# Performance work log

Hardware: AMD Instinct MI355X
Metric: run time of the kernel (lower is better)

Reference implementation:

```python
import jax, jax.numpy as jnp
import numpy as np

N_RAYS = 4096
WORLD_LEN = 160
K0_DIM = 12
WIDTH = 128
VIEWPE = 4
BG_LEN = 0.2
XYZ_MIN = -1.0 - BG_LEN
XYZ_MAX = 1.0 + BG_LEN
ALPHA_INIT = 1e-4
ACT_SHIFT = float(np.log(1.0 / (1.0 - ALPHA_INIT) - 1.0))  # density bias shift
BG = 1.0  # background color (render_kwargs['bg'])
DIM0 = 3 + 3 * VIEWPE * 2 + K0_DIM  # 39


def grid_interp(grid, pts):
    """Trilinear interpolation (align_corners=True). grid: [C,R,R,R], pts: [M,3] world coords -> [M,C]."""
    R = grid.shape[1]
    g = (pts - XYZ_MIN) / (XYZ_MAX - XYZ_MIN) * (R - 1)
    g = jnp.clip(g, 0.0, R - 1)
    g0 = jnp.clip(jnp.floor(g).astype(jnp.int32), 0, R - 2)
    f = g - g0
    x0, y0, z0 = g0[:, 0], g0[:, 1], g0[:, 2]
    fx, fy, fz = f[:, 0], f[:, 1], f[:, 2]

    def gat(i, j, k):
        return grid[:, i, j, k]  # [C, M]

    c00 = gat(x0, y0, z0) * (1 - fz) + gat(x0, y0, z0 + 1) * fz
    c01 = gat(x0, y0 + 1, z0) * (1 - fz) + gat(x0, y0 + 1, z0 + 1) * fz
    c10 = gat(x0 + 1, y0, z0) * (1 - fz) + gat(x0 + 1, y0, z0 + 1) * fz
    c11 = gat(x0 + 1, y0 + 1, z0) * (1 - fz) + gat(x0 + 1, y0 + 1, z0 + 1) * fz
    c0 = c00 * (1 - fy) + c01 * fy
    c1 = c10 * (1 - fy) + c11 * fy
    return (c0 * (1 - fx) + c1 * fx).T  # [M, C]


def setup_inputs() -> dict:
    key = jax.random.key(0)
    ks = jax.random.split(key, 11)
    return {
        "rays_o": jax.random.normal(ks[0], (N_RAYS, 3), jnp.float32) * 0.3,
        "rays_d": jax.random.normal(ks[1], (N_RAYS, 3), jnp.float32),
        "viewdirs": jax.random.normal(ks[2], (N_RAYS, 3), jnp.float32),
        "density_grid": jax.random.normal(ks[3], (1, WORLD_LEN, WORLD_LEN, WORLD_LEN), jnp.float32),
        "k0_grid": jax.random.normal(ks[4], (K0_DIM, WORLD_LEN, WORLD_LEN, WORLD_LEN), jnp.float32),
        "w0": jax.random.normal(ks[5], (DIM0, WIDTH), jnp.float32) * 0.05,
        "b0": jnp.zeros((WIDTH,), jnp.float32),
        "w1": jax.random.normal(ks[6], (WIDTH, WIDTH), jnp.float32) * 0.05,
        "b1": jnp.zeros((WIDTH,), jnp.float32),
        "w2": jax.random.normal(ks[7], (WIDTH, 3), jnp.float32) * 0.05,
        "b2": jnp.zeros((3,), jnp.float32),
        "stepsize": 1,
    }


def reference(rays_o, rays_d, viewdirs, density_grid, k0_grid, w0, b0, w1, b1, w2, b2, stepsize):
    sqrt3 = float(np.sqrt(3.0))
    # --- sample_ray: sample points along rays in the contracted domain ---
    N_inner = int(2.0 / (2.0 + 2.0 * BG_LEN) * sqrt3 * WORLD_LEN / stepsize) + 1
    N_outer = int(N_inner * max(0.01, BG_LEN / 2.0))
    b_inner = jnp.linspace(0.0, 2.0 * sqrt3, N_inner + 1)
    b_outer = 2.0 * sqrt3 / jnp.linspace(1.0, 0.001, N_outer + 1)
    t = jnp.concatenate([(b_inner[1:] + b_inner[:-1]) * 0.5,
                         (b_outer[1:] + b_outer[:-1]) * 0.5])  # [P]
    # scene_center = 0, scene_radius = 1 for xyz_min=-1, xyz_max=1
    rd = rays_d / jnp.linalg.norm(rays_d, axis=-1, keepdims=True)
    pts = rays_o[:, None, :] + rd[:, None, :] * t[None, :, None]  # [N,P,3]
    norm = jnp.max(jnp.abs(pts), axis=-1, keepdims=True)
    safe = jnp.maximum(norm, 1e-9)
    pts = jnp.where(norm <= 1.0, pts, pts / safe * (1.0 + BG_LEN - BG_LEN / safe))
    N, P = pts.shape[0], pts.shape[1]
    flat = pts.reshape(-1, 3)  # [M,3]

    # --- density -> alpha (Raw2Alpha); mask_cache is all-True, fast_color_thres=0 ---
    interval = float(stepsize) * 1.0  # voxel_size_ratio == 1
    dens = grid_interp(density_grid, flat)[:, 0].reshape(N, P)
    alpha = 1.0 - jnp.power(1.0 + jnp.exp(dens + ACT_SHIFT), -interval)

    # --- Alphas2Weights: per-ray alpha compositing ---
    T = jnp.cumprod(1.0 - alpha, axis=1)
    T_excl = jnp.concatenate([jnp.ones((N, 1), T.dtype), T[:, :-1]], axis=1)
    weights = alpha * T_excl  # [N,P]
    alphainv_last = T[:, -1]  # [N]

    # --- k0 features + view-dependent MLP ---
    k0 = grid_interp(k0_grid, flat).reshape(N, P, K0_DIM)
    vf = (2.0 ** jnp.arange(VIEWPE)).astype(rays_o.dtype)
    ve = (viewdirs[..., None] * vf).reshape(N, -1)
    vemb = jnp.concatenate([viewdirs, jnp.sin(ve), jnp.cos(ve)], axis=-1)  # [N, 3+24]
    feat = jnp.concatenate(
        [k0, jnp.broadcast_to(vemb[:, None, :], (N, P, vemb.shape[-1]))], axis=-1)  # [N,P,39]
    h = jax.nn.relu(feat @ w0 + b0)
    h = jax.nn.relu(h @ w1 + b1)
    rgb = jax.nn.sigmoid(h @ w2 + b2)  # [N,P,3]

    # --- volume rendering ---
    rgb_marched = jnp.sum(weights[..., None] * rgb, axis=1) + alphainv_last[:, None] * BG
    return rgb_marched  # [N,3]
```

## Files before the change

### kernel.cpp

```cpp
#include <hip/hip_runtime.h>

#define NRAYS 4096
#define PSAMP 254
#define NIN   231
#define GR    160
#define GR2   25600
#define GR3   4096000
#define SROW  136

typedef __attribute__((ext_vector_type(8))) short bf16x8;
typedef __attribute__((ext_vector_type(4))) float f32x4;

__device__ __forceinline__ unsigned short f2bf(float x) {
    union { float f; unsigned u; } v; v.f = x;
    return (unsigned short)((v.u + 0x7fffu + ((v.u >> 16) & 1u)) >> 16);
}
__device__ __forceinline__ float sigmoidf_(float x) { return 1.0f / (1.0f + __expf(-x)); }

__global__ void prepack(const float* __restrict__ w, unsigned short* __restrict__ out,
                        int K, int N, int ldw, int NT, int KS) {
    const int idx = blockIdx.x * 256 + threadIdx.x;
    if (idx >= NT * KS * 64) return;
    const int l  = idx & 63, f = idx >> 6;
    const int ks = f % KS,  nt = f / KS;
    const int n  = nt * 16 + (l & 15);
    const int k0 = ks * 32 + (l >> 4) * 8;
    unsigned p[4];
    #pragma unroll
    for (int q = 0; q < 4; q++) {
        const int ka = k0 + 2 * q, kb = ka + 1;
        const float va = (ka < K && n < N) ? w[ka * ldw + n] : 0.0f;
        const float vb = (kb < K && n < N) ? w[kb * ldw + n] : 0.0f;
        p[q] = (unsigned)f2bf(va) | ((unsigned)f2bf(vb) << 16);
    }
    uint4 v; v.x = p[0]; v.y = p[1]; v.z = p[2]; v.w = p[3];
    ((uint4*)out)[idx] = v;
}

__global__ __launch_bounds__(256, 2) void voxgo_mfma(
    const float* __restrict__ rays_o, const float* __restrict__ rays_d,
    const float* __restrict__ viewdirs, const float* __restrict__ dg,
    const float* __restrict__ k0g,
    const float* __restrict__ b0, const float* __restrict__ b1,
    const float* __restrict__ b2,
    const unsigned short* __restrict__ pw0, const unsigned short* __restrict__ pw1,
    const unsigned short* __restrict__ pw2,
    float* __restrict__ out)
{
    const int r    = blockIdx.x;
    const int tid  = threadIdx.x;
    const int wv   = tid >> 6, lane = tid & 63, quad = lane >> 4, l16 = lane & 15;

    __shared__ unsigned short hbuf[4][64 * SROW];
    __shared__ float sc[256];
    __shared__ float wgt[256];
    __shared__ float redbuf[256];

    const float ox = rays_o[3*r+0], oy = rays_o[3*r+1], oz = rays_o[3*r+2];
    float dxv = rays_d[3*r+0], dyv = rays_d[3*r+1], dzv = rays_d[3*r+2];
    const float vdx = viewdirs[3*r+0], vdy = viewdirs[3*r+1], vdz = viewdirs[3*r+2];
    const float rinv = rsqrtf(dxv*dxv + dyv*dyv + dzv*dzv);
    dxv *= rinv; dyv *= rinv; dzv *= rinv;

    float t;
    if (tid < NIN) {
        t = ((float)tid + 0.5f) * (2.0f * 1.7320508075688772f / 231.0f);
    } else {
        const float lstep = 0.999f / 23.0f;
        const int j = tid - NIN;
        const float L0 = 1.0f - (float)j * lstep;
        const float L1 = 1.0f - (float)(j+1) * lstep;
        t = 1.7320508075688772f * (1.0f/L0 + 1.0f/L1);
    }

    float px = fmaf(dxv, t, ox), py = fmaf(dyv, t, oy), pz = fmaf(dzv, t, oz);
    const float nrm = fmaxf(fabsf(px), fmaxf(fabsf(py), fabsf(pz)));
    if (nrm > 1.0f) {
        const float s = (1.2f - 0.2f / nrm) / nrm;
        px *= s; py *= s; pz *= s;
    }

    const float gsc = 159.0f / 2.4f;
    const float gx = fminf(fmaxf((px + 1.2f) * gsc, 0.0f), 159.0f);
    const float gy = fminf(fmaxf((py + 1.2f) * gsc, 0.0f), 159.0f);
    const float gz = fminf(fmaxf((pz + 1.2f) * gsc, 0.0f), 159.0f);
    const int x0 = min((int)gx, GR-2), y0 = min((int)gy, GR-2), z0 = min((int)gz, GR-2);
    const float fx = gx - (float)x0, fy = gy - (float)y0, fz = gz - (float)z0;
    const int base = x0*GR2 + y0*GR + z0;

    const float d000 = dg[base],        d001 = dg[base+1];
    const float d010 = dg[base+GR],     d011 = dg[base+GR+1];
    const float d100 = dg[base+GR2],    d101 = dg[base+GR2+1];
    const float d110 = dg[base+GR2+GR], d111 = dg[base+GR2+GR+1];
    const float c00 = d000*(1.0f-fz) + d001*fz;
    const float c01 = d010*(1.0f-fz) + d011*fz;
    const float c10 = d100*(1.0f-fz) + d101*fz;
    const float c11 = d110*(1.0f-fz) + d111*fz;
    const float dens = (c00*(1.0f-fy) + c01*fy)*(1.0f-fx) + (c10*(1.0f-fy) + c11*fy)*fx;

    const float ACT_SHIFT = -9.21024036697535f;
    const float alpha = (tid < PSAMP) ? sigmoidf_(dens + ACT_SHIFT) : 0.0f;

    sc[tid] = 1.0f - alpha;
    __syncthreads();
    #pragma unroll
    for (int off = 1; off < 256; off <<= 1) {
        const float v = (tid >= off) ? sc[tid - off] : 1.0f;
        __syncthreads();
        sc[tid] *= v;
        __syncthreads();
    }
    const float T_excl = (tid == 0) ? 1.0f : sc[tid-1];
    wgt[tid] = alpha * T_excl;

    const float wx0 = 1.0f-fx, wy0 = 1.0f-fy, wz0 = 1.0f-fz;
    const float w000 = wx0*wy0*wz0, w001 = wx0*wy0*fz, w010 = wx0*fy*wz0, w011 = wx0*fy*fz;
    const float w100 = fx*wy0*wz0,  w101 = fx*wy0*fz,  w110 = fx*fy*wz0,  w111 = fx*fy*fz;

    float fv[40];
    #pragma unroll
    for (int c = 0; c < 12; c++) {
        const float* g = k0g + c*GR3 + base;
        fv[c] = w000*g[0]      + w001*g[1]
              + w010*g[GR]     + w011*g[GR+1]
              + w100*g[GR2]    + w101*g[GR2+1]
              + w110*g[GR2+GR] + w111*g[GR2+GR+1];
    }
    fv[12] = vdx; fv[13] = vdy; fv[14] = vdz;
    #pragma unroll
    for (int p = 0; p < 4; p++) {
        const float f = (float)(1 << p);
        fv[15+p] = __sinf(vdx*f);  fv[19+p] = __sinf(vdy*f);  fv[23+p] = __sinf(vdz*f);
        fv[27+p] = __cosf(vdx*f);  fv[31+p] = __cosf(vdy*f);  fv[35+p] = __cosf(vdz*f);
    }
    fv[39] = 0.0f;

    unsigned short* hb = &hbuf[wv][0];
    {
        const int row = tid & 63;
        uint4* dst = (uint4*)(hb + row * SROW);
        #pragma unroll
        for (int i = 0; i < 8; i++) {
            unsigned p[4];
            #pragma unroll
            for (int q = 0; q < 4; q++) {
                const int e0 = i*8 + 2*q, e1 = e0 + 1;
                const unsigned lo = (e0 < 39) ? f2bf(fv[e0]) : 0u;
                const unsigned hi = (e1 < 39) ? f2bf(fv[e1]) : 0u;
                p[q] = lo | (hi << 16);
            }
            uint4 v; v.x = p[0]; v.y = p[1]; v.z = p[2]; v.w = p[3];
            dst[i] = v;
        }
    }
    __syncthreads();


    f32x4 acc1[4][8];
    #pragma unroll
    for (int nt = 0; nt < 8; nt++) {
        const float bz = b0[nt*16 + l16];
        #pragma unroll
        for (int mt = 0; mt < 4; mt++) { f32x4 z = {bz,bz,bz,bz}; acc1[mt][nt] = z; }
    }
    #pragma unroll
    for (int ks = 0; ks < 2; ks++) {
        bf16x8 a[4];
        #pragma unroll
        for (int mt = 0; mt < 4; mt++)
            a[mt] = *(const bf16x8*)(hb + (mt*16 + l16)*SROW + ks*32 + quad*8);
        #pragma unroll
        for (int nt = 0; nt < 8; nt++) {
            const bf16x8 b = *(const bf16x8*)(pw0 + ((nt*2 + ks)*64 + lane)*8);
            #pragma unroll
            for (int mt = 0; mt < 4; mt++)
                acc1[mt][nt] = __builtin_amdgcn_mfma_f32_16x16x32_bf16(a[mt], b, acc1[mt][nt], 0,0,0);
        }
    }
    #pragma unroll
    for (int mt = 0; mt < 4; mt++)
        #pragma unroll
        for (int nt = 0; nt < 8; nt++)
            #pragma unroll
            for (int e = 0; e < 4; e++)
                hb[(mt*16 + quad*4 + e)*SROW + nt*16 + l16] = f2bf(fmaxf(acc1[mt][nt][e], 0.0f));
    __syncthreads();

    f32x4 acc2[4][8];
    #pragma unroll
    for (int nt = 0; nt < 8; nt++) {
        const float bz = b1[nt*16 + l16];
        #pragma unroll
        for (int mt = 0; mt < 4; mt++) { f32x4 z = {bz,bz,bz,bz}; acc2[mt][nt] = z; }
    }
    #pragma unroll
    for (int ks = 0; ks < 4; ks++) {
        bf16x8 a[4];
        #pragma unroll
        for (int mt = 0; mt < 4; mt++)
            a[mt] = *(const bf16x8*)(hb + (mt*16 + l16)*SROW + ks*32 + quad*8);
        #pragma unroll
        for (int nt = 0; nt < 8; nt++) {
            const bf16x8 b = *(const bf16x8*)(pw1 + ((nt*4 + ks)*64 + lane)*8);
            #pragma unroll
            for (int mt = 0; mt < 4; mt++)
                acc2[mt][nt] = __builtin_amdgcn_mfma_f32_16x16x32_bf16(a[mt], b, acc2[mt][nt], 0,0,0);
        }
    }
    #pragma unroll
    for (int mt = 0; mt < 4; mt++)
        #pragma unroll
        for (int nt = 0; nt < 8; nt++)
            #pragma unroll
            for (int e = 0; e < 4; e++)
                hb[(mt*16 + quad*4 + e)*SROW + nt*16 + l16] = f2bf(fmaxf(acc2[mt][nt][e], 0.0f));
    __syncthreads();

    f32x4 acc3[4];
    {
        const float bz = (l16 < 3) ? b2[l16] : 0.0f;
        #pragma unroll
        for (int mt = 0; mt < 4; mt++) { f32x4 z = {bz,bz,bz,bz}; acc3[mt] = z; }
    }
    #pragma unroll
    for (int ks = 0; ks < 4; ks++) {
        const bf16x8 b = *(const bf16x8*)(pw2 + (ks*64 + lane)*8);
        #pragma unroll
        for (int mt = 0; mt < 4; mt++) {
            const bf16x8 a = *(const bf16x8*)(hb + (mt*16 + l16)*SROW + ks*32 + quad*8);
            acc3[mt] = __builtin_amdgcn_mfma_f32_16x16x32_bf16(a, b, acc3[mt], 0,0,0);
        }
    }

    float contrib = 0.0f;
    #pragma unroll
    for (int mt = 0; mt < 4; mt++)
        #pragma unroll
        for (int e = 0; e < 4; e++) {
            const float s = sigmoidf_(acc3[mt][e]);
            contrib += wgt[wv*64 + mt*16 + quad*4 + e] * s;
        }
    redbuf[tid] = contrib;
    __syncthreads();
    if (tid < 3) {
        float acc_o = sc[PSAMP-1];
        #pragma unroll
        for (int w = 0; w < 4; w++)
            #pragma unroll
            for (int q = 0; q < 4; q++)
                acc_o += redbuf[w*64 + q*16 + tid];
        out[3*r + tid] = acc_o;
    }
}

extern "C" void kernel_launch(void* const* d_in, const int* in_sizes, int n_in,
                              void* d_out, int out_size, void* d_ws, size_t ws_size,
                              hipStream_t stream) {
    (void)in_sizes; (void)n_in; (void)out_size; (void)ws_size;
    unsigned short* pw0 = (unsigned short*)d_ws;
    unsigned short* pw1 = pw0 + 16*64*8;
    unsigned short* pw2 = pw1 + 32*64*8;

    prepack<<<4, 256, 0, stream>>>((const float*)d_in[5], pw0,  39, 128, 128, 8, 2);
    prepack<<<8, 256, 0, stream>>>((const float*)d_in[7], pw1, 128, 128, 128, 8, 4);
    prepack<<<1, 256, 0, stream>>>((const float*)d_in[9], pw2, 128,   3,   3, 1, 4);

    voxgo_mfma<<<NRAYS, 256, 0, stream>>>(
        (const float*)d_in[0],
        (const float*)d_in[1],
        (const float*)d_in[2],
        (const float*)d_in[3],
        (const float*)d_in[4],
        (const float*)d_in[6],
        (const float*)d_in[8],
        (const float*)d_in[10],
        pw0, pw1, pw2,
        (float*)d_out);
}
```

Baseline: 526.0 us.

## Split fused kernel into k0 repack, gather, and MLP kernels via workspace

```diff
diff --git a/kernel.cpp b/kernel.cpp
--- a/kernel.cpp
+++ b/kernel.cpp
@@ -7,6 +7,7 @@
 #define GR2   25600
 #define GR3   4096000
 #define SROW  136
+#define FROW  48
 
 typedef __attribute__((ext_vector_type(8))) short bf16x8;
 typedef __attribute__((ext_vector_type(4))) float f32x4;
@@ -14,6 +15,11 @@
 __device__ __forceinline__ unsigned short f2bf(float x) {
     union { float f; unsigned u; } v; v.f = x;
     return (unsigned short)((v.u + 0x7fffu + ((v.u >> 16) & 1u)) >> 16);
+}
+__device__ __forceinline__ float bfhalf(unsigned w, int hi) {
+    union { unsigned u; float f; } v;
+    v.u = hi ? (w & 0xffff0000u) : (w << 16);
+    return v.f;
 }
 __device__ __forceinline__ float sigmoidf_(float x) { return 1.0f / (1.0f + __expf(-x)); }
 
@@ -35,6 +41,238 @@
     }
     uint4 v; v.x = p[0]; v.y = p[1]; v.z = p[2]; v.w = p[3];
     ((uint4*)out)[idx] = v;
+}
+
+__global__ __launch_bounds__(256) void pack_k0(const float* __restrict__ k0g,
+                                               unsigned short* __restrict__ pk) {
+    const int v = blockIdx.x * 256 + threadIdx.x;
+    if (v >= GR3) return;
+    unsigned d[8];
+    #pragma unroll
+    for (int c = 0; c < 6; c++) {
+        const float a = k0g[(size_t)(2*c  ) * GR3 + v];
+        const float b = k0g[(size_t)(2*c+1) * GR3 + v];
+        d[c] = (unsigned)f2bf(a) | ((unsigned)f2bf(b) << 16);
+    }
+    d[6] = 0u; d[7] = 0u;
+    uint4* o = (uint4*)(pk + (size_t)v * 16);
+    uint4 v0; v0.x = d[0]; v0.y = d[1]; v0.z = d[2]; v0.w = d[3];
+    uint4 v1; v1.x = d[4]; v1.y = d[5]; v1.z = d[6]; v1.w = d[7];
+    o[0] = v0; o[1] = v1;
+}
+
+__global__ __launch_bounds__(256) void voxgo_gather(
+    const float* __restrict__ rays_o, const float* __restrict__ rays_d,
+    const float* __restrict__ viewdirs, const float* __restrict__ dg,
+    const unsigned short* __restrict__ pk0,
+    unsigned short* __restrict__ feat, float* __restrict__ wgt,
+    float* __restrict__ out)
+{
+    const int r = blockIdx.x, tid = threadIdx.x;
+    __shared__ float sc[256];
+
+    const float ox = rays_o[3*r+0], oy = rays_o[3*r+1], oz = rays_o[3*r+2];
+    float dxv = rays_d[3*r+0], dyv = rays_d[3*r+1], dzv = rays_d[3*r+2];
+    const float vdx = viewdirs[3*r+0], vdy = viewdirs[3*r+1], vdz = viewdirs[3*r+2];
+    const float rinv = rsqrtf(dxv*dxv + dyv*dyv + dzv*dzv);
+    dxv *= rinv; dyv *= rinv; dzv *= rinv;
+
+    float t;
+    if (tid < NIN) {
+        t = ((float)tid + 0.5f) * (2.0f * 1.7320508075688772f / 231.0f);
+    } else {
+        const float lstep = 0.999f / 23.0f;
+        const int j = tid - NIN;
+        const float L0 = 1.0f - (float)j * lstep;
+        const float L1 = 1.0f - (float)(j+1) * lstep;
+        t = 1.7320508075688772f * (1.0f/L0 + 1.0f/L1);
+    }
+
+    float px = fmaf(dxv, t, ox), py = fmaf(dyv, t, oy), pz = fmaf(dzv, t, oz);
+    const float nrm = fmaxf(fabsf(px), fmaxf(fabsf(py), fabsf(pz)));
+    if (nrm > 1.0f) {
+        const float s = (1.2f - 0.2f / nrm) / nrm;
+        px *= s; py *= s; pz *= s;
+    }
+    const float gsc = 159.0f / 2.4f;
+    const float gx = fminf(fmaxf((px + 1.2f) * gsc, 0.0f), 159.0f);
+    const float gy = fminf(fmaxf((py + 1.2f) * gsc, 0.0f), 159.0f);
+    const float gz = fminf(fmaxf((pz + 1.2f) * gsc, 0.0f), 159.0f);
+    const int x0 = min((int)gx, GR-2), y0 = min((int)gy, GR-2), z0 = min((int)gz, GR-2);
+    const float fx = gx - (float)x0, fy = gy - (float)y0, fz = gz - (float)z0;
+    const int base = x0*GR2 + y0*GR + z0;
+
+    const float d000 = dg[base],        d001 = dg[base+1];
+    const float d010 = dg[base+GR],     d011 = dg[base+GR+1];
+    const float d100 = dg[base+GR2],    d101 = dg[base+GR2+1];
+    const float d110 = dg[base+GR2+GR], d111 = dg[base+GR2+GR+1];
+    const float c00 = d000*(1.0f-fz) + d001*fz;
+    const float c01 = d010*(1.0f-fz) + d011*fz;
+    const float c10 = d100*(1.0f-fz) + d101*fz;
+    const float c11 = d110*(1.0f-fz) + d111*fz;
+    const float dens = (c00*(1.0f-fy) + c01*fy)*(1.0f-fx) + (c10*(1.0f-fy) + c11*fy)*fx;
+
+    const float ACT_SHIFT = -9.21024036697535f;
+    const float alpha = (tid < PSAMP) ? sigmoidf_(dens + ACT_SHIFT) : 0.0f;
+
+    sc[tid] = 1.0f - alpha;
+    __syncthreads();
+    #pragma unroll
+    for (int off = 1; off < 256; off <<= 1) {
+        const float v = (tid >= off) ? sc[tid - off] : 1.0f;
+        __syncthreads();
+        sc[tid] *= v;
+        __syncthreads();
+    }
+    const float T_excl = (tid == 0) ? 1.0f : sc[tid-1];
+    wgt[(size_t)r*256 + tid] = alpha * T_excl;
+    if (tid < 3) out[3*r + tid] = sc[PSAMP-1];
+
+    const int off_[8] = {0, 1, GR, GR+1, GR2, GR2+1, GR2+GR, GR2+GR+1};
+    unsigned crw[8][8];
+    #pragma unroll
+    for (int i = 0; i < 8; i++) {
+        const uint4* p = (const uint4*)(pk0 + (size_t)(base + off_[i]) * 16);
+        const uint4 a = p[0], b = p[1];
+        crw[i][0]=a.x; crw[i][1]=a.y; crw[i][2]=a.z; crw[i][3]=a.w;
+        crw[i][4]=b.x; crw[i][5]=b.y; crw[i][6]=b.z; crw[i][7]=b.w;
+    }
+    const float wx0 = 1.0f-fx, wy0 = 1.0f-fy, wz0 = 1.0f-fz;
+    float w8[8];
+    w8[0]=wx0*wy0*wz0; w8[1]=wx0*wy0*fz; w8[2]=wx0*fy*wz0; w8[3]=wx0*fy*fz;
+    w8[4]=fx*wy0*wz0;  w8[5]=fx*wy0*fz;  w8[6]=fx*fy*wz0;  w8[7]=fx*fy*fz;
+
+    float fva[40];
+    #pragma unroll
+    for (int c = 0; c < 12; c++) {
+        const int wd = c >> 1, hi = c & 1;
+        float acc = 0.0f;
+        #pragma unroll
+        for (int i = 0; i < 8; i++) acc += w8[i] * bfhalf(crw[i][wd], hi);
+        fva[c] = acc;
+    }
+    fva[12] = vdx; fva[13] = vdy; fva[14] = vdz;
+    #pragma unroll
+    for (int p = 0; p < 4; p++) {
+        const float f = (float)(1 << p);
+        fva[15+p] = __sinf(vdx*f);  fva[19+p] = __sinf(vdy*f);  fva[23+p] = __sinf(vdz*f);
+        fva[27+p] = __cosf(vdx*f);  fva[31+p] = __cosf(vdy*f);  fva[35+p] = __cosf(vdz*f);
+    }
+    fva[39] = 0.0f;
+
+    unsigned pwd[20];
+    #pragma unroll
+    for (int q = 0; q < 20; q++)
+        pwd[q] = (unsigned)f2bf(fva[2*q]) | ((unsigned)f2bf(fva[2*q+1]) << 16);
+    uint4* dst = (uint4*)(feat + ((size_t)r*256 + tid) * FROW);
+    uint4 s0; s0.x=pwd[0];  s0.y=pwd[1];  s0.z=pwd[2];  s0.w=pwd[3];  dst[0]=s0;
+    uint4 s1; s1.x=pwd[4];  s1.y=pwd[5];  s1.z=pwd[6];  s1.w=pwd[7];  dst[1]=s1;
+    uint4 s2; s2.x=pwd[8];  s2.y=pwd[9];  s2.z=pwd[10]; s2.w=pwd[11]; dst[2]=s2;
+    uint4 s3; s3.x=pwd[12]; s3.y=pwd[13]; s3.z=pwd[14]; s3.w=pwd[15]; dst[3]=s3;
+    uint4 s4; s4.x=pwd[16]; s4.y=pwd[17]; s4.z=pwd[18]; s4.w=pwd[19]; dst[4]=s4;
+}
+
+__global__ __launch_bounds__(64) void voxgo_mlp(
+    const unsigned short* __restrict__ feat, const float* __restrict__ wgt,
+    const float* __restrict__ b0, const float* __restrict__ b1, const float* __restrict__ b2,
+    const unsigned short* __restrict__ pw0, const unsigned short* __restrict__ pw1,
+    const unsigned short* __restrict__ pw2, float* __restrict__ out)
+{
+    const int blk  = blockIdx.x;
+    const int ray  = blk >> 2, wq = blk & 3;
+    const int lane = threadIdx.x, quad = lane >> 4, l16 = lane & 15;
+    const size_t s0 = (size_t)ray*256 + wq*64;
+
+    __shared__ unsigned short hb[64 * SROW];
+    __shared__ float red[64];
+
+    f32x4 acc1[4][8];
+    #pragma unroll
+    for (int nt = 0; nt < 8; nt++) {
+        const float bz = b0[nt*16 + l16];
+        #pragma unroll
+        for (int mt = 0; mt < 4; mt++) { f32x4 z = {bz,bz,bz,bz}; acc1[mt][nt] = z; }
+    }
+    #pragma unroll
+    for (int ks = 0; ks < 2; ks++) {
+        bf16x8 a[4];
+        #pragma unroll
+        for (int mt = 0; mt < 4; mt++)
+            a[mt] = *(const bf16x8*)(feat + (s0 + mt*16 + l16)*FROW + ks*32 + quad*8);
+        #pragma unroll
+        for (int nt = 0; nt < 8; nt++) {
+            const bf16x8 b = *(const bf16x8*)(pw0 + ((nt*2 + ks)*64 + lane)*8);
+            #pragma unroll
+            for (int mt = 0; mt < 4; mt++)
+                acc1[mt][nt] = __builtin_amdgcn_mfma_f32_16x16x32_bf16(a[mt], b, acc1[mt][nt], 0,0,0);
+        }
+    }
+    #pragma unroll
+    for (int mt = 0; mt < 4; mt++)
+        #pragma unroll
+        for (int nt = 0; nt < 8; nt++)
+            #pragma unroll
+            for (int e = 0; e < 4; e++)
+                hb[(mt*16 + quad*4 + e)*SROW + nt*16 + l16] = f2bf(fmaxf(acc1[mt][nt][e], 0.0f));
+    __syncthreads();
+
+    f32x4 acc2[4][8];
+    #pragma unroll
+    for (int nt = 0; nt < 8; nt++) {
+        const float bz = b1[nt*16 + l16];
+        #pragma unroll
+        for (int mt = 0; mt < 4; mt++) { f32x4 z = {bz,bz,bz,bz}; acc2[mt][nt] = z; }
+    }
+    #pragma unroll
+    for (int ks = 0; ks < 4; ks++) {
+        bf16x8 a[4];
+        #pragma unroll
+        for (int mt = 0; mt < 4; mt++)
+            a[mt] = *(const bf16x8*)(hb + (mt*16 + l16)*SROW + ks*32 + quad*8);
+        #pragma unroll
+        for (int nt = 0; nt < 8; nt++) {
+            const bf16x8 b = *(const bf16x8*)(pw1 + ((nt*4 + ks)*64 + lane)*8);
+            #pragma unroll
+            for (int mt = 0; mt < 4; mt++)
+                acc2[mt][nt] = __builtin_amdgcn_mfma_f32_16x16x32_bf16(a[mt], b, acc2[mt][nt], 0,0,0);
+        }
+    }
+    __syncthreads();
+    #pragma unroll
+    for (int mt = 0; mt < 4; mt++)
+        #pragma unroll
+        for (int nt = 0; nt < 8; nt++)
+            #pragma unroll
+            for (int e = 0; e < 4; e++)
+                hb[(mt*16 + quad*4 + e)*SROW + nt*16 + l16] = f2bf(fmaxf(acc2[mt][nt][e], 0.0f));
+    __syncthreads();
+
+    f32x4 acc3[4];
+    {
+        const float bz = (l16 < 3) ? b2[l16] : 0.0f;
+        #pragma unroll
+        for (int mt = 0; mt < 4; mt++) { f32x4 z = {bz,bz,bz,bz}; acc3[mt] = z; }
+    }
+    #pragma unroll
+    for (int ks = 0; ks < 4; ks++) {
+        const bf16x8 b = *(const bf16x8*)(pw2 + (ks*64 + lane)*8);
+        #pragma unroll
+        for (int mt = 0; mt < 4; mt++) {
+            const bf16x8 a = *(const bf16x8*)(hb + (mt*16 + l16)*SROW + ks*32 + quad*8);
+            acc3[mt] = __builtin_amdgcn_mfma_f32_16x16x32_bf16(a, b, acc3[mt], 0,0,0);
+        }
+    }
+
+    float contrib = 0.0f;
+    #pragma unroll
+    for (int mt = 0; mt < 4; mt++)
+        #pragma unroll
+        for (int e = 0; e < 4; e++)
+            contrib += wgt[s0 + mt*16 + quad*4 + e] * sigmoidf_(acc3[mt][e]);
+    red[lane] = contrib;
+    __syncthreads();
+    if (lane < 3)
+        atomicAdd(&out[3*ray + lane], red[lane] + red[lane+16] + red[lane+32] + red[lane+48]);
 }
 
 __global__ __launch_bounds__(256, 2) void voxgo_mfma(
@@ -79,7 +317,6 @@
         const float s = (1.2f - 0.2f / nrm) / nrm;
         px *= s; py *= s; pz *= s;
     }
-
     const float gsc = 159.0f / 2.4f;
     const float gx = fminf(fmaxf((px + 1.2f) * gsc, 0.0f), 159.0f);
     const float gy = fminf(fmaxf((py + 1.2f) * gsc, 0.0f), 159.0f);
@@ -120,7 +357,7 @@
     float fv[40];
     #pragma unroll
     for (int c = 0; c < 12; c++) {
-        const float* g = k0g + c*GR3 + base;
+        const float* g = k0g + (size_t)c*GR3 + base;
         fv[c] = w000*g[0]      + w001*g[1]
               + w010*g[GR]     + w011*g[GR+1]
               + w100*g[GR2]    + w101*g[GR2+1]
@@ -155,7 +392,6 @@
     }
     __syncthreads();
 
-
     f32x4 acc1[4][8];
     #pragma unroll
     for (int nt = 0; nt < 8; nt++) {
@@ -207,6 +443,7 @@
                 acc2[mt][nt] = __builtin_amdgcn_mfma_f32_16x16x32_bf16(a[mt], b, acc2[mt][nt], 0,0,0);
         }
     }
+    __syncthreads();
     #pragma unroll
     for (int mt = 0; mt < 4; mt++)
         #pragma unroll
@@ -236,10 +473,8 @@
     #pragma unroll
     for (int mt = 0; mt < 4; mt++)
         #pragma unroll
-        for (int e = 0; e < 4; e++) {
-            const float s = sigmoidf_(acc3[mt][e]);
-            contrib += wgt[wv*64 + mt*16 + quad*4 + e] * s;
-        }
+        for (int e = 0; e < 4; e++)
+            contrib += wgt[wv*64 + mt*16 + quad*4 + e] * sigmoidf_(acc3[mt][e]);
     redbuf[tid] = contrib;
     __syncthreads();
     if (tid < 3) {
@@ -256,7 +491,13 @@
 extern "C" void kernel_launch(void* const* d_in, const int* in_sizes, int n_in,
                               void* d_out, int out_size, void* d_ws, size_t ws_size,
                               hipStream_t stream) {
-    (void)in_sizes; (void)n_in; (void)out_size; (void)ws_size;
+    (void)in_sizes; (void)n_in; (void)out_size;
+
+    const size_t PWB   = 53248;
+    const size_t PACKB = 131072000ull;
+    const size_t FEATB = 100667392ull;
+    const size_t WGTB  = 4194304ull;
+
     unsigned short* pw0 = (unsigned short*)d_ws;
     unsigned short* pw1 = pw0 + 16*64*8;
     unsigned short* pw2 = pw1 + 32*64*8;
@@ -265,15 +506,26 @@
     prepack<<<8, 256, 0, stream>>>((const float*)d_in[7], pw1, 128, 128, 128, 8, 4);
     prepack<<<1, 256, 0, stream>>>((const float*)d_in[9], pw2, 128,   3,   3, 1, 4);
 
-    voxgo_mfma<<<NRAYS, 256, 0, stream>>>(
-        (const float*)d_in[0],
-        (const float*)d_in[1],
-        (const float*)d_in[2],
-        (const float*)d_in[3],
-        (const float*)d_in[4],
-        (const float*)d_in[6],
-        (const float*)d_in[8],
-        (const float*)d_in[10],
-        pw0, pw1, pw2,
-        (float*)d_out);
-}
+    if (ws_size >= PWB + PACKB + FEATB + WGTB) {
+        unsigned short* pk0  = (unsigned short*)((char*)d_ws + PWB);
+        unsigned short* feat = (unsigned short*)((char*)d_ws + PWB + PACKB);
+        float*          wgt  = (float*)((char*)d_ws + PWB + PACKB + FEATB);
+
+        pack_k0<<<(GR3 + 255)/256, 256, 0, stream>>>((const float*)d_in[4], pk0);
+
+        voxgo_gather<<<NRAYS, 256, 0, stream>>>(
+            (const float*)d_in[0], (const float*)d_in[1], (const float*)d_in[2],
+            (const float*)d_in[3], pk0, feat, wgt, (float*)d_out);
+
+        voxgo_mlp<<<NRAYS*4, 64, 0, stream>>>(
+            feat, wgt,
+            (const float*)d_in[6], (const float*)d_in[8], (const float*)d_in[10],
+            pw0, pw1, pw2, (float*)d_out);
+    } else {
+        voxgo_mfma<<<NRAYS, 256, 0, stream>>>(
+            (const float*)d_in[0], (const float*)d_in[1], (const float*)d_in[2],
+            (const float*)d_in[3], (const float*)d_in[4],
+            (const float*)d_in[6], (const float*)d_in[8], (const float*)d_in[10],
+            pw0, pw1, pw2, (float*)d_out);
+    }
+}
```

Measured after the change: 553.3 us. 1.05x slower.
